# Kernel tuning notes

Hardware: AMD Instinct MI355X
Metric: run time of the kernel (lower is better)

Reference implementation:

```python
import jax, jax.numpy as jnp
import numpy as np
import math

N_OBS, DIM_IN, DIM_HIDDEN = 2048, 64, 1024
LENGTHSCALE = 1.0


def setup_inputs() -> dict:
    key = jax.random.key(0)
    kx, kw, kb = jax.random.split(key, 3)
    x = jax.random.normal(kx, (N_OBS, DIM_IN), dtype=jnp.float32)
    # buffer w ~ Normal(0, 1/lengthscale), b ~ Uniform(0, 2*pi)
    w = jax.random.normal(kw, (DIM_HIDDEN, DIM_IN), dtype=jnp.float32) / LENGTHSCALE
    b = jax.random.uniform(kb, (DIM_HIDDEN,), dtype=jnp.float32, minval=0.0, maxval=2.0 * math.pi)
    return {"x": x, "w": w, "b": b}


def reference(x, w, b):
    """compute_Ax: analytic jacobian of hidden_features + per-dim Gram matrices.

    hidden h = sqrt(2/K) * cos(x @ w.T + b)
    jacobian J[n,k,d] = -sqrt(2/K) * sin(z[n,k]) * w[k,d]
    A_d[k,l] = (1/n) * sum_n J[n,k,d] * J[n,l,d]
             = (1/n) * (S^T S)[k,l] * w[k,d] * w[l,d],  S = -sqrt(2/K) sin(z)
    Returns A stacked: (dim_in, K, K).
    """
    n = x.shape[0]
    K = w.shape[0]
    scale = math.sqrt(2.0 / K)
    z = x @ w.T + b  # (n, K)
    s = (-scale) * jnp.sin(z)  # (n, K)
    M = (s.T @ s) / n  # (K, K) shared Gram of sin-activations
    # A[d,k,l] = M[k,l] * w[k,d] * w[l,d]
    A = jnp.einsum('kl,kd,ld->dkl', M, w, w)
    return A
```

## Files before the change

kernel.cpp:

```cpp
#include <hip/hip_runtime.h>
#include <math.h>

#define N_OBS   2048
#define DIM_IN  64
#define K_HID   1024

typedef unsigned short ushort_t;
typedef __attribute__((ext_vector_type(8))) short bf16x8;
typedef __attribute__((ext_vector_type(4))) float f32x4;

__device__ __forceinline__ ushort_t f2bf(float f) {
    unsigned int u = __float_as_uint(f);
    u += 0x7FFF + ((u >> 16) & 1);
    return (ushort_t)(u >> 16);
}

__global__ __launch_bounds__(256) void rff_transpose_w(
    const float* __restrict__ w, float* __restrict__ wt) {
    int t = blockIdx.x * 256 + threadIdx.x;
    int l = t >> 6;
    int d = t & 63;
    wt[d * K_HID + l] = w[t];
}

__global__ __launch_bounds__(256) void rff_compute_s(
    const float* __restrict__ x, const float* __restrict__ w,
    const float* __restrict__ b, ushort_t* __restrict__ sT) {
    __shared__ float xs[16][64];
    __shared__ float wT[64][65];

    const int t  = threadIdx.x;
    const int k0 = blockIdx.x * 64;
    const int n0 = blockIdx.y * 16;

    {
        int r = t >> 4, c = (t & 15) * 4;
        *(float4*)&xs[r][c] = *(const float4*)(x + (n0 + r) * DIM_IN + c);
    }
#pragma unroll
    for (int i = 0; i < 4; ++i) {
        int r = (t >> 4) + 16 * i, c = (t & 15) * 4;
        float4 v = *(const float4*)(w + (k0 + r) * DIM_IN + c);
        wT[c + 0][r] = v.x; wT[c + 1][r] = v.y;
        wT[c + 2][r] = v.z; wT[c + 3][r] = v.w;
    }
    __syncthreads();

    const int k  = t & 63;
    const int nb = t >> 6;
    const float bk = b[k0 + k];
    float z[4];
#pragma unroll
    for (int i = 0; i < 4; ++i) z[i] = bk;

    for (int d4 = 0; d4 < 64; d4 += 4) {
        float xv[4][4];
#pragma unroll
        for (int i = 0; i < 4; ++i)
            *(float4*)xv[i] = *(const float4*)&xs[nb * 4 + i][d4];
#pragma unroll
        for (int j = 0; j < 4; ++j) {
            const float wv = wT[d4 + j][k];
#pragma unroll
            for (int i = 0; i < 4; ++i) z[i] += xv[i][j] * wv;
        }
    }

    const float scale = 0.04419417382415922f;
    ushort4 ov;
    ov.x = f2bf(-scale * __sinf(z[0]));
    ov.y = f2bf(-scale * __sinf(z[1]));
    ov.z = f2bf(-scale * __sinf(z[2]));
    ov.w = f2bf(-scale * __sinf(z[3]));
    *(ushort4*)(sT + (size_t)(k0 + k) * N_OBS + n0 + nb * 4) = ov;
}

__global__ __launch_bounds__(256) void rff_gram_mfma(
    const ushort_t* __restrict__ sT, float* __restrict__ M) {
    __shared__ ushort_t ldsA[64 * 64];
    __shared__ ushort_t ldsB[64 * 64];

    const int t    = threadIdx.x;
    const int lane = t & 63;
    const int wv   = t >> 6;
    const int wr   = wv >> 1, wc = wv & 1;
    const int k0   = blockIdx.y * 64, l0 = blockIdx.x * 64;

    f32x4 acc[2][2];
#pragma unroll
    for (int a = 0; a < 2; ++a)
#pragma unroll
        for (int bb = 0; bb < 2; ++bb)
            acc[a][bb] = (f32x4){0.f, 0.f, 0.f, 0.f};

    const int srow = t >> 3;
    const int scol = (t & 7) * 8;

    for (int n0 = 0; n0 < N_OBS; n0 += 64) {
        bf16x8 ra[2], rb[2];
#pragma unroll
        for (int i = 0; i < 2; ++i) {
            ra[i] = *(const bf16x8*)(sT + (size_t)(k0 + i * 32 + srow) * N_OBS + n0 + scol);
            rb[i] = *(const bf16x8*)(sT + (size_t)(l0 + i * 32 + srow) * N_OBS + n0 + scol);
        }
        __syncthreads();
#pragma unroll
        for (int i = 0; i < 2; ++i) {
            *(bf16x8*)(ldsA + i * 2048 + t * 8) = ra[i];
            *(bf16x8*)(ldsB + i * 2048 + t * 8) = rb[i];
        }
        __syncthreads();

#pragma unroll
        for (int ks = 0; ks < 2; ++ks) {
            bf16x8 af[2], bfr[2];
#pragma unroll
            for (int a = 0; a < 2; ++a) {
                af[a]  = *(const bf16x8*)(ldsA + (wr * 32 + a * 16 + (lane & 15)) * 64
                                          + ks * 32 + (lane >> 4) * 8);
                bfr[a] = *(const bf16x8*)(ldsB + (wc * 32 + a * 16 + (lane & 15)) * 64
                                          + ks * 32 + (lane >> 4) * 8);
            }
#pragma unroll
            for (int a = 0; a < 2; ++a)
#pragma unroll
                for (int bb = 0; bb < 2; ++bb)
                    acc[a][bb] = __builtin_amdgcn_mfma_f32_16x16x32_bf16(
                        af[a], bfr[bb], acc[a][bb], 0, 0, 0);
        }
    }

    const float inv_n = 1.0f / (float)N_OBS;
    const int col = lane & 15;
    const int rq  = (lane >> 4) * 4;
#pragma unroll
    for (int a = 0; a < 2; ++a)
#pragma unroll
        for (int bb = 0; bb < 2; ++bb)
#pragma unroll
            for (int r = 0; r < 4; ++r) {
                const int row = k0 + wr * 32 + a * 16 + rq + r;
                const int cl  = l0 + wc * 32 + bb * 16 + col;
                M[(size_t)row * K_HID + cl] = acc[a][bb][r] * inv_n;
            }
}

__global__ __launch_bounds__(256) void rff_expand_A(
    const float* __restrict__ M, const float* __restrict__ wt,
    float* __restrict__ out) {
    const int kg = blockIdx.x;
    const int d  = blockIdx.y;
    const int t  = threadIdx.x;

    const float4 wl = *(const float4*)(wt + d * K_HID + t * 4);
    const int k0 = kg * 4;
#pragma unroll
    for (int i = 0; i < 4; ++i) {
        const int k = k0 + i;
        const float wk = wt[d * K_HID + k];
        const float4 mv = *(const float4*)(M + (size_t)k * K_HID + t * 4);
        float4 o;
        o.x = mv.x * wk * wl.x;
        o.y = mv.y * wk * wl.y;
        o.z = mv.z * wk * wl.z;
        o.w = mv.w * wk * wl.w;
        *(float4*)(out + ((size_t)(d * K_HID + k)) * K_HID + t * 4) = o;
    }
}

extern "C" void kernel_launch(void* const* d_in, const int* in_sizes, int n_in,
                              void* d_out, int out_size, void* d_ws, size_t ws_size,
                              hipStream_t stream) {
    const float* x = (const float*)d_in[0];
    const float* w = (const float*)d_in[1];
    const float* b = (const float*)d_in[2];
    float* out = (float*)d_out;

    char* ws = (char*)d_ws;
    ushort_t* sT_buf = (ushort_t*)ws;
    float*    M_buf  = (float*)(ws + (size_t)4 * 1024 * 1024);
    float*    wt_buf = (float*)(ws + (size_t)8 * 1024 * 1024);

    rff_transpose_w<<<dim3((K_HID * DIM_IN) / 256), 256, 0, stream>>>(w, wt_buf);
    rff_compute_s<<<dim3(K_HID / 64, N_OBS / 16), 256, 0, stream>>>(x, w, b, sT_buf);
    rff_gram_mfma<<<dim3(K_HID / 64, K_HID / 64), 256, 0, stream>>>(sT_buf, M_buf);
    rff_expand_A<<<dim3(K_HID / 4, DIM_IN), 256, 0, stream>>>(M_buf, wt_buf, out);
}
```

Baseline: 301.4 us.

## Split-K gram with async LDS double buffering, fuse transpose, nontemporal expand stores

Fuses the weight transpose into the sin-activation kernel and splits the Gram GEMM over the observation axis into two partial products, followed by a small reduce kernel. The Gram loop now stages tiles with direct global-to-LDS loads into double-buffered, XOR-swizzled shared memory to overlap loads with MFMA. The output expansion kernel processes 16 rows per block and uses nontemporal stores for the large 256 MB output. This adds an extra kernel and an 8 MB partial buffer round-trip in exchange for more parallelism and better store behaviour.

```diff
diff --git a/kernel.cpp b/kernel.cpp
--- a/kernel.cpp
+++ b/kernel.cpp
@@ -4,6 +4,8 @@
 #define N_OBS   2048
 #define DIM_IN  64
 #define K_HID   1024
+#define NSPLIT  2
+#define NT_CHUNK ((N_OBS / NSPLIT) / 64)
 
 typedef unsigned short ushort_t;
 typedef __attribute__((ext_vector_type(8))) short bf16x8;
@@ -15,17 +17,15 @@
     return (ushort_t)(u >> 16);
 }
 
-__global__ __launch_bounds__(256) void rff_transpose_w(
-    const float* __restrict__ w, float* __restrict__ wt) {
-    int t = blockIdx.x * 256 + threadIdx.x;
-    int l = t >> 6;
-    int d = t & 63;
-    wt[d * K_HID + l] = w[t];
-}
+#define GLD_LDS16(g, l)                                                   \
+    __builtin_amdgcn_global_load_lds(                                     \
+        (const __attribute__((address_space(1))) void*)(g),               \
+        (__attribute__((address_space(3))) void*)(l), 16, 0, 0)
 
 __global__ __launch_bounds__(256) void rff_compute_s(
     const float* __restrict__ x, const float* __restrict__ w,
-    const float* __restrict__ b, ushort_t* __restrict__ sT) {
+    const float* __restrict__ b, ushort_t* __restrict__ sT,
+    float* __restrict__ wt) {
     __shared__ float xs[16][64];
     __shared__ float wT[64][65];
 
@@ -48,6 +48,15 @@
 
     const int k  = t & 63;
     const int nb = t >> 6;
+
+    if (blockIdx.y == 0) {
+#pragma unroll
+        for (int dd = 0; dd < 16; ++dd) {
+            const int d = nb + dd * 4;
+            wt[d * K_HID + k0 + k] = wT[d][k];
+        }
+    }
+
     const float bk = b[k0 + k];
     float z[4];
 #pragma unroll
@@ -75,16 +84,33 @@
     *(ushort4*)(sT + (size_t)(k0 + k) * N_OBS + n0 + nb * 4) = ov;
 }
 
+__device__ __forceinline__ void stage_tiles(
+    const ushort_t* __restrict__ sT, ushort_t* lA, ushort_t* lB,
+    int k0, int l0, int ncol0, int wv, int srow, int sslot) {
+#pragma unroll
+    for (int j = 0; j < 2; ++j) {
+        const int c = wv * 2 + j;
+        const ushort_t* gA = sT + (size_t)(k0 + c * 8 + srow) * N_OBS + ncol0 + sslot * 8;
+        const ushort_t* gB = sT + (size_t)(l0 + c * 8 + srow) * N_OBS + ncol0 + sslot * 8;
+        GLD_LDS16(gA, lA + c * 512);
+        GLD_LDS16(gB, lB + c * 512);
+    }
+}
+
 __global__ __launch_bounds__(256) void rff_gram_mfma(
-    const ushort_t* __restrict__ sT, float* __restrict__ M) {
-    __shared__ ushort_t ldsA[64 * 64];
-    __shared__ ushort_t ldsB[64 * 64];
+    const ushort_t* __restrict__ sT, float* __restrict__ Mp) {
+    __shared__ ushort_t ldsA[2][64 * 64];
+    __shared__ ushort_t ldsB[2][64 * 64];
 
     const int t    = threadIdx.x;
     const int lane = t & 63;
     const int wv   = t >> 6;
     const int wr   = wv >> 1, wc = wv & 1;
     const int k0   = blockIdx.y * 64, l0 = blockIdx.x * 64;
+    const int nbase = blockIdx.z * (N_OBS / NSPLIT);
+
+    const int srow  = lane >> 3;
+    const int sslot = (lane & 7) ^ srow;
 
     f32x4 acc[2][2];
 #pragma unroll
@@ -93,33 +119,26 @@
         for (int bb = 0; bb < 2; ++bb)
             acc[a][bb] = (f32x4){0.f, 0.f, 0.f, 0.f};
 
-    const int srow = t >> 3;
-    const int scol = (t & 7) * 8;
-
-    for (int n0 = 0; n0 < N_OBS; n0 += 64) {
-        bf16x8 ra[2], rb[2];
-#pragma unroll
-        for (int i = 0; i < 2; ++i) {
-            ra[i] = *(const bf16x8*)(sT + (size_t)(k0 + i * 32 + srow) * N_OBS + n0 + scol);
-            rb[i] = *(const bf16x8*)(sT + (size_t)(l0 + i * 32 + srow) * N_OBS + n0 + scol);
-        }
-        __syncthreads();
-#pragma unroll
-        for (int i = 0; i < 2; ++i) {
-            *(bf16x8*)(ldsA + i * 2048 + t * 8) = ra[i];
-            *(bf16x8*)(ldsB + i * 2048 + t * 8) = rb[i];
-        }
-        __syncthreads();
-
+    const int rlo = lane & 15;
+    const int hi  = lane >> 4;
+    const int rx  = rlo & 7;
+
+    stage_tiles(sT, &ldsA[0][0], &ldsB[0][0], k0, l0, nbase, wv, srow, sslot);
+    __syncthreads();
+
+    int cur = 0;
+    for (int it = 0; it < NT_CHUNK; ++it) {
+        if (it + 1 < NT_CHUNK)
+            stage_tiles(sT, &ldsA[cur ^ 1][0], &ldsB[cur ^ 1][0],
+                        k0, l0, nbase + (it + 1) * 64, wv, srow, sslot);
 #pragma unroll
         for (int ks = 0; ks < 2; ++ks) {
+            const int slot = (ks * 4 + hi) ^ rx;
             bf16x8 af[2], bfr[2];
 #pragma unroll
             for (int a = 0; a < 2; ++a) {
-                af[a]  = *(const bf16x8*)(ldsA + (wr * 32 + a * 16 + (lane & 15)) * 64
-                                          + ks * 32 + (lane >> 4) * 8);
-                bfr[a] = *(const bf16x8*)(ldsB + (wc * 32 + a * 16 + (lane & 15)) * 64
-                                          + ks * 32 + (lane >> 4) * 8);
+                af[a]  = *(const bf16x8*)(&ldsA[cur][(wr * 32 + a * 16 + rlo) * 64 + slot * 8]);
+                bfr[a] = *(const bf16x8*)(&ldsB[cur][(wc * 32 + a * 16 + rlo) * 64 + slot * 8]);
             }
 #pragma unroll
             for (int a = 0; a < 2; ++a)
@@ -128,9 +147,11 @@
                     acc[a][bb] = __builtin_amdgcn_mfma_f32_16x16x32_bf16(
                         af[a], bfr[bb], acc[a][bb], 0, 0, 0);
         }
-    }
-
-    const float inv_n = 1.0f / (float)N_OBS;
+        __syncthreads();
+        cur ^= 1;
+    }
+
+    float* Mz = Mp + (size_t)blockIdx.z * K_HID * K_HID;
     const int col = lane & 15;
     const int rq  = (lane >> 4) * 4;
 #pragma unroll
@@ -141,8 +162,20 @@
             for (int r = 0; r < 4; ++r) {
                 const int row = k0 + wr * 32 + a * 16 + rq + r;
                 const int cl  = l0 + wc * 32 + bb * 16 + col;
-                M[(size_t)row * K_HID + cl] = acc[a][bb][r] * inv_n;
+                Mz[(size_t)row * K_HID + cl] = acc[a][bb][r];
             }
+}
+
+__global__ __launch_bounds__(256) void rff_reduce_M(
+    const float* __restrict__ Mp, float* __restrict__ M) {
+    const int i = (blockIdx.x * 256 + threadIdx.x) * 4;
+    const f32x4 a = *(const f32x4*)(Mp + i);
+    const f32x4 c = *(const f32x4*)(Mp + (size_t)K_HID * K_HID + i);
+    const float inv_n = 1.0f / (float)N_OBS;
+    f32x4 o;
+#pragma unroll
+    for (int j = 0; j < 4; ++j) o[j] = (a[j] + c[j]) * inv_n;
+    *(f32x4*)(M + i) = o;
 }
 
 __global__ __launch_bounds__(256) void rff_expand_A(
@@ -152,19 +185,18 @@
     const int d  = blockIdx.y;
     const int t  = threadIdx.x;
 
-    const float4 wl = *(const float4*)(wt + d * K_HID + t * 4);
-    const int k0 = kg * 4;
-#pragma unroll
-    for (int i = 0; i < 4; ++i) {
+    const f32x4 wl = *(const f32x4*)(wt + d * K_HID + t * 4);
+    const int k0 = kg * 16;
+#pragma unroll
+    for (int i = 0; i < 16; ++i) {
         const int k = k0 + i;
         const float wk = wt[d * K_HID + k];
-        const float4 mv = *(const float4*)(M + (size_t)k * K_HID + t * 4);
-        float4 o;
-        o.x = mv.x * wk * wl.x;
-        o.y = mv.y * wk * wl.y;
-        o.z = mv.z * wk * wl.z;
-        o.w = mv.w * wk * wl.w;
-        *(float4*)(out + ((size_t)(d * K_HID + k)) * K_HID + t * 4) = o;
+        const f32x4 mv = *(const f32x4*)(M + (size_t)k * K_HID + t * 4);
+        f32x4 o;
+#pragma unroll
+        for (int j = 0; j < 4; ++j) o[j] = mv[j] * wk * wl[j];
+        __builtin_nontemporal_store(
+            o, (f32x4*)(out + ((size_t)(d * K_HID + k)) * K_HID + t * 4));
     }
 }
 
@@ -178,11 +210,12 @@
 
     char* ws = (char*)d_ws;
     ushort_t* sT_buf = (ushort_t*)ws;
-    float*    M_buf  = (float*)(ws + (size_t)4 * 1024 * 1024);
-    float*    wt_buf = (float*)(ws + (size_t)8 * 1024 * 1024);
-
-    rff_transpose_w<<<dim3((K_HID * DIM_IN) / 256), 256, 0, stream>>>(w, wt_buf);
-    rff_compute_s<<<dim3(K_HID / 64, N_OBS / 16), 256, 0, stream>>>(x, w, b, sT_buf);
-    rff_gram_mfma<<<dim3(K_HID / 64, K_HID / 64), 256, 0, stream>>>(sT_buf, M_buf);
-    rff_expand_A<<<dim3(K_HID / 4, DIM_IN), 256, 0, stream>>>(M_buf, wt_buf, out);
-}
+    float*    Mp_buf = (float*)(ws + (size_t)4  * 1024 * 1024);
+    float*    M_buf  = (float*)(ws + (size_t)12 * 1024 * 1024);
+    float*    wt_buf = (float*)(ws + (size_t)16 * 1024 * 1024);
+
+    rff_compute_s<<<dim3(K_HID / 64, N_OBS / 16), 256, 0, stream>>>(x, w, b, sT_buf, wt_buf);
+    rff_gram_mfma<<<dim3(K_HID / 64, K_HID / 64, NSPLIT), 256, 0, stream>>>(sT_buf, Mp_buf);
+    rff_reduce_M<<<dim3(K_HID * K_HID / 1024), 256, 0, stream>>>(Mp_buf, M_buf);
+    rff_expand_A<<<dim3(K_HID / 16, DIM_IN), 256, 0, stream>>>(M_buf, wt_buf, out);
+}
```

New measurement: 301.8 us. Within noise of the previous version (+0.1%).
